# Optimization experiments

Hardware: AMD Instinct MI355X
Metric: run time of the kernel (lower is better)

Reference implementation:

```python
import jax, jax.numpy as jnp
import numpy as np

B, T, C, H = 2, 4096, 512, 8
HD = C // H  # head_dim = 64


def setup_inputs() -> dict:
    key = jax.random.key(0)
    ks = jax.random.split(key, 5)
    s = 0.02
    return {
        "x": jax.random.normal(ks[0], (B, T, C), dtype=jnp.float32),
        "Wqkv": jax.random.normal(ks[1], (C, 3 * C), dtype=jnp.float32) * s,
        "bqkv": jax.random.normal(ks[2], (3 * C,), dtype=jnp.float32) * s,
        "Wproj": jax.random.normal(ks[3], (C, C), dtype=jnp.float32) * s,
        "bproj": jax.random.normal(ks[4], (C,), dtype=jnp.float32) * s,
    }


def reference(x, Wqkv, bqkv, Wproj, bproj):
    b, t, c = x.shape
    qkv = x @ Wqkv + bqkv                      # [B,T,3C]
    q, k, v = jnp.split(qkv, 3, axis=-1)
    # [B,T,C] -> [B,H,T,HD]
    q = q.reshape(b, t, H, HD).transpose(0, 2, 1, 3)
    k = k.reshape(b, t, H, HD).transpose(0, 2, 1, 3)
    v = v.reshape(b, t, H, HD).transpose(0, 2, 1, 3)
    att = jnp.einsum("bhqd,bhkd->bhqk", q, k) / jnp.sqrt(jnp.float32(HD))
    causal = jnp.tril(jnp.ones((t, t), dtype=bool))
    att = jnp.where(causal, att, -jnp.inf)
    att = jax.nn.softmax(att, axis=-1)
    y = jnp.einsum("bhqk,bhkd->bhqd", att, v)  # [B,H,T,HD]
    y = y.transpose(0, 2, 1, 3).reshape(b, t, c)
    return y @ Wproj + bproj
```

## Files before the change

### kernel.cpp

```cpp
#include <hip/hip_runtime.h>
#include <math.h>

#define NB 2
#define NT 4096
#define NC 512
#define NH 8
#define ND 64
#define N3C (3*NC)

typedef __attribute__((ext_vector_type(8))) __bf16 bf16x8;
typedef __attribute__((ext_vector_type(4))) __bf16 bf16x4;
typedef __attribute__((ext_vector_type(4))) float  f32x4;

__global__ __launch_bounds__(256) void cvt_bf16_kernel(
    const float* __restrict__ x, __bf16* __restrict__ xb, int n)
{
    const int i = (blockIdx.x * 256 + threadIdx.x) << 3;
    if (i < n) {
        float4 a = *(const float4*)(x + i);
        float4 b = *(const float4*)(x + i + 4);
        bf16x8 o;
        o[0] = (__bf16)a.x; o[1] = (__bf16)a.y; o[2] = (__bf16)a.z; o[3] = (__bf16)a.w;
        o[4] = (__bf16)b.x; o[5] = (__bf16)b.y; o[6] = (__bf16)b.z; o[7] = (__bf16)b.w;
        *(bf16x8*)(xb + i) = o;
    }
}

__global__ __launch_bounds__(256) void transpose_cvt_kernel(
    const float* __restrict__ W, __bf16* __restrict__ Wt, int K, int N)
{
    __shared__ float T[64][65];
    const int n0 = blockIdx.x << 6, k0 = blockIdx.y << 6;
    const int tx = threadIdx.x & 15, ty = threadIdx.x >> 4;
#pragma unroll
    for (int i = 0; i < 4; ++i) {
        const int r = ty + (i << 4);
        float4 v = *(const float4*)(W + (size_t)(k0 + r) * N + n0 + (tx << 2));
        T[r][(tx << 2) + 0] = v.x;
        T[r][(tx << 2) + 1] = v.y;
        T[r][(tx << 2) + 2] = v.z;
        T[r][(tx << 2) + 3] = v.w;
    }
    __syncthreads();
#pragma unroll
    for (int i = 0; i < 4; ++i) {
        const int nr = ty + (i << 4);
        bf16x4 o;
        o[0] = (__bf16)T[(tx << 2) + 0][nr];
        o[1] = (__bf16)T[(tx << 2) + 1][nr];
        o[2] = (__bf16)T[(tx << 2) + 2][nr];
        o[3] = (__bf16)T[(tx << 2) + 3][nr];
        *(bf16x4*)(Wt + (size_t)(n0 + nr) * K + k0 + (tx << 2)) = o;
    }
}

__global__ __launch_bounds__(256) void gemm_bf16_kernel(
    const __bf16* __restrict__ A, const __bf16* __restrict__ Bt,
    const float* __restrict__ bias, void* __restrict__ Cout,
    int M, int N, int K, int out_bf16)
{
    __shared__ __bf16 As[128][40];
    __shared__ __bf16 Bs[128][40];

    const int tid  = threadIdx.x;
    const int w    = tid >> 6, lane = tid & 63;
    const int g    = lane >> 4, n = lane & 15;
    const int wr   = (w >> 1) << 6;
    const int wc   = (w & 1) << 6;
    const int m0   = blockIdx.y << 7, n0 = blockIdx.x << 7;

    const int sr = tid >> 1;
    const int sh = (tid & 1) << 4;
    const __bf16* ap = A  + (size_t)(m0 + sr) * K + sh;
    const __bf16* bp = Bt + (size_t)(n0 + sr) * K + sh;

    f32x4 acc[4][4];
#pragma unroll
    for (int i = 0; i < 4; ++i)
#pragma unroll
        for (int j = 0; j < 4; ++j) acc[i][j] = (f32x4){0.f, 0.f, 0.f, 0.f};

    bf16x8 a0 = *(const bf16x8*)ap;
    bf16x8 a1 = *(const bf16x8*)(ap + 8);
    bf16x8 b0 = *(const bf16x8*)bp;
    bf16x8 b1 = *(const bf16x8*)(bp + 8);

    const int ksteps = K >> 5;
    for (int ks = 0; ks < ksteps; ++ks) {
        __syncthreads();
        *(bf16x8*)&As[sr][sh]     = a0;
        *(bf16x8*)&As[sr][sh + 8] = a1;
        *(bf16x8*)&Bs[sr][sh]     = b0;
        *(bf16x8*)&Bs[sr][sh + 8] = b1;
        __syncthreads();

        if (ks + 1 < ksteps) {
            const int ko = (ks + 1) << 5;
            a0 = *(const bf16x8*)(ap + ko);
            a1 = *(const bf16x8*)(ap + ko + 8);
            b0 = *(const bf16x8*)(bp + ko);
            b1 = *(const bf16x8*)(bp + ko + 8);
        }

        bf16x8 af[4], bf[4];
#pragma unroll
        for (int i = 0; i < 4; ++i) {
            af[i] = *(const bf16x8*)&As[wr + (i << 4) + n][g << 3];
            bf[i] = *(const bf16x8*)&Bs[wc + (i << 4) + n][g << 3];
        }
#pragma unroll
        for (int i = 0; i < 4; ++i)
#pragma unroll
            for (int j = 0; j < 4; ++j)
                acc[i][j] = __builtin_amdgcn_mfma_f32_16x16x32_bf16(af[i], bf[j], acc[i][j], 0, 0, 0);
    }

#pragma unroll
    for (int j = 0; j < 4; ++j) {
        const int colg = n0 + wc + (j << 4) + n;
        const float bb = bias[colg];
#pragma unroll
        for (int i = 0; i < 4; ++i) {
#pragma unroll
            for (int reg = 0; reg < 4; ++reg) {
                const int rowg = m0 + wr + (i << 4) + (g << 2) + reg;
                const float v = acc[i][j][reg] + bb;
                if (out_bf16)
                    ((__bf16*)Cout)[(size_t)rowg * N + colg] = (__bf16)v;
                else
                    ((float*)Cout)[(size_t)rowg * N + colg] = v;
            }
        }
    }
}

__global__ __launch_bounds__(512) void attn_kernel(
    const __bf16* __restrict__ qkv, __bf16* __restrict__ out)
{
    __shared__ __align__(16) unsigned char SMEM[36352];
    __bf16 (*QPs)[72] = (__bf16(*)[72])SMEM;
    __bf16 (*Ks)[72]  = (__bf16(*)[72])(SMEM + 18432);
    __bf16 (*Vt)[68]  = (__bf16(*)[68])(SMEM + 27648);

    const int tid  = threadIdx.x;
    const int xi   = blockIdx.x;
    const int bh   = blockIdx.y;
    const int qb   = (bh < 8) ? (31 - xi) : xi;
    const int b    = bh >> 3, h = bh & 7;
    const int qr0  = qb << 7;
    const size_t base = (size_t)b * NT * N3C;
    const int col  = h * ND;

    const int w    = tid >> 6;
    const int lane = tid & 63;
    const int g    = lane >> 4;
    const int n    = lane & 15;
    const int qg   = w >> 1;
    const int kh   = w & 1;
    const int qrow0 = qg << 5;
    const int kcol0 = kh << 5;
    const int sw   = (g ^ (n >> 2)) << 3;

    const int kr = tid >> 3;
    const int kc = (tid & 7) << 3;
    const int vd = lane;
    const int vk = w << 2;

    const __bf16* kptr = qkv + base + NC + col + kc;
    const __bf16* vptr = qkv + base + 2 * NC + col + vd;

#pragma unroll
    for (int i = 0; i < 2; ++i) {
        const int r = kr + (i << 6);
        bf16x8 v = *(const bf16x8*)(qkv + base + (size_t)(qr0 + r) * N3C + col + kc);
        bf16x8 q;
#pragma unroll
        for (int j = 0; j < 8; ++j) q[j] = (__bf16)(0.125f * (float)v[j]);
        *(bf16x8*)&QPs[r][kc] = q;
    }
    __syncthreads();

    bf16x8 qf[2][2];
#pragma unroll
    for (int qt = 0; qt < 2; ++qt)
#pragma unroll
        for (int hh = 0; hh < 2; ++hh)
            qf[qt][hh] = *(const bf16x8*)&QPs[qrow0 + (qt << 4) + n][(hh << 5) + (g << 3)];

    bf16x8 ones;
#pragma unroll
    for (int j = 0; j < 8; ++j) ones[j] = (__bf16)1.0f;

    f32x4 O[2][4];
#pragma unroll
    for (int qt = 0; qt < 2; ++qt)
#pragma unroll
        for (int dt = 0; dt < 4; ++dt) O[qt][dt] = (f32x4){0.f, 0.f, 0.f, 0.f};
    f32x4 L[2] = {{0.f,0.f,0.f,0.f},{0.f,0.f,0.f,0.f}};

    bf16x8 kreg = *(const bf16x8*)(kptr + (size_t)kr * N3C);
    __bf16 vreg[8];
#pragma unroll
    for (int j = 0; j < 4; ++j) {
        vreg[j]     = vptr[(size_t)(vk + j) * N3C];
        vreg[4 + j] = vptr[(size_t)(vk + 32 + j) * N3C];
    }

    const int ntiles = (qb << 1) + 2;
    for (int jt = 0; jt < ntiles; ++jt) {
        __syncthreads();
        *(bf16x8*)&Ks[kr][kc] = kreg;
        {
            bf16x4 va, vb;
#pragma unroll
            for (int j = 0; j < 4; ++j) { va[j] = vreg[j]; vb[j] = vreg[4 + j]; }
            *(bf16x4*)&Vt[vd][vk]      = va;
            *(bf16x4*)&Vt[vd][vk + 32] = vb;
        }
        __syncthreads();

        if (jt + 1 < ntiles) {
            const int kr1 = (jt + 1) << 6;
            kreg = *(const bf16x8*)(kptr + (size_t)(kr1 + kr) * N3C);
#pragma unroll
            for (int j = 0; j < 4; ++j) {
                vreg[j]     = vptr[(size_t)(kr1 + vk + j) * N3C];
                vreg[4 + j] = vptr[(size_t)(kr1 + vk + 32 + j) * N3C];
            }
        }

        f32x4 S[2][2];
#pragma unroll
        for (int t = 0; t < 2; ++t) {
            const bf16x8 k0 = *(const bf16x8*)&Ks[kcol0 + (t << 4) + n][(g << 3)];
            const bf16x8 k1 = *(const bf16x8*)&Ks[kcol0 + (t << 4) + n][32 + (g << 3)];
#pragma unroll
            for (int qt = 0; qt < 2; ++qt) {
                f32x4 a = {0.f, 0.f, 0.f, 0.f};
                a = __builtin_amdgcn_mfma_f32_16x16x32_bf16(qf[qt][0], k0, a, 0, 0, 0);
                a = __builtin_amdgcn_mfma_f32_16x16x32_bf16(qf[qt][1], k1, a, 0, 0, 0);
                S[qt][t] = a;
            }
        }

        if (jt >= (qb << 1)) {
#pragma unroll
            for (int qt = 0; qt < 2; ++qt)
#pragma unroll
                for (int t = 0; t < 2; ++t)
#pragma unroll
                    for (int reg = 0; reg < 4; ++reg) {
                        const int kg = (jt << 6) + kcol0 + (t << 4) + n;
                        const int qgl = qr0 + qrow0 + (qt << 4) + (g << 2) + reg;
                        if (kg > qgl) S[qt][t][reg] = -INFINITY;
                    }
        }

#pragma unroll
        for (int qt = 0; qt < 2; ++qt)
#pragma unroll
            for (int t = 0; t < 2; ++t)
#pragma unroll
                for (int reg = 0; reg < 4; ++reg)
                    QPs[qrow0 + (qt << 4) + (g << 2) + reg]
                       [kcol0 + (((t << 4) + n) ^ (g << 3))] =
                        (__bf16)__expf(S[qt][t][reg]);

        bf16x8 vf[4];
#pragma unroll
        for (int dt = 0; dt < 4; ++dt) {
            const int vr = (dt << 4) + n;
            const bf16x4 lo = *(const bf16x4*)&Vt[vr][kcol0 + (g << 3)];
            const bf16x4 hi = *(const bf16x4*)&Vt[vr][kcol0 + (g << 3) + 4];
#pragma unroll
            for (int j = 0; j < 4; ++j) { vf[dt][j] = lo[j]; vf[dt][4 + j] = hi[j]; }
        }

#pragma unroll
        for (int qt = 0; qt < 2; ++qt) {
            const bf16x8 p = *(const bf16x8*)&QPs[qrow0 + (qt << 4) + n][kcol0 + sw];
            L[qt] = __builtin_amdgcn_mfma_f32_16x16x32_bf16(p, ones, L[qt], 0, 0, 0);
#pragma unroll
            for (int dt = 0; dt < 4; ++dt)
                O[qt][dt] = __builtin_amdgcn_mfma_f32_16x16x32_bf16(p, vf[dt], O[qt][dt], 0, 0, 0);
        }
    }

    __syncthreads();
    float* red = (float*)SMEM;
    if (kh == 1) {
#pragma unroll
        for (int qt = 0; qt < 2; ++qt)
#pragma unroll
            for (int reg = 0; reg < 4; ++reg) {
                const int qlx = qrow0 + (qt << 4) + (g << 2) + reg;
#pragma unroll
                for (int dt = 0; dt < 4; ++dt)
                    red[qlx * 64 + (dt << 4) + n] = O[qt][dt][reg];
                if (n == 0) red[8192 + qlx] = L[qt][reg];
            }
    }
    __syncthreads();
    if (kh == 0) {
#pragma unroll
        for (int qt = 0; qt < 2; ++qt)
#pragma unroll
            for (int reg = 0; reg < 4; ++reg) {
                const int qlx = qrow0 + (qt << 4) + (g << 2) + reg;
                const float inv = 1.0f / (L[qt][reg] + red[8192 + qlx]);
                const size_t row = (size_t)b * NT + qr0 + qlx;
#pragma unroll
                for (int dt = 0; dt < 4; ++dt)
                    out[row * NC + col + (dt << 4) + n] =
                        (__bf16)((O[qt][dt][reg] + red[qlx * 64 + (dt << 4) + n]) * inv);
            }
    }
}

extern "C" void kernel_launch(void* const* d_in, const int* in_sizes, int n_in,
                              void* d_out, int out_size, void* d_ws, size_t ws_size,
                              hipStream_t stream)
{
    const float* x     = (const float*)d_in[0];
    const float* Wqkv  = (const float*)d_in[1];
    const float* bqkv  = (const float*)d_in[2];
    const float* Wproj = (const float*)d_in[3];
    const float* bproj = (const float*)d_in[4];
    float* out = (float*)d_out;

    char* ws = (char*)d_ws;
    __bf16* xb     = (__bf16*)(ws);
    __bf16* qkvb   = (__bf16*)(ws + 8388608);
    __bf16* attb   = (__bf16*)(ws + 33554432);
    __bf16* wqkvt  = (__bf16*)(ws + 41943040);
    __bf16* wprojt = (__bf16*)(ws + 43515904);

    cvt_bf16_kernel<<<dim3(2048), dim3(256), 0, stream>>>(x, xb, NB * NT * NC);
    transpose_cvt_kernel<<<dim3(N3C / 64, NC / 64), dim3(256), 0, stream>>>(
        Wqkv, wqkvt, NC, N3C);
    transpose_cvt_kernel<<<dim3(NC / 64, NC / 64), dim3(256), 0, stream>>>(
        Wproj, wprojt, NC, NC);

    gemm_bf16_kernel<<<dim3(N3C / 128, (NB * NT) / 128), dim3(256), 0, stream>>>(
        xb, wqkvt, bqkv, qkvb, NB * NT, N3C, NC, 1);

    attn_kernel<<<dim3(NT / 128, NB * NH), dim3(512), 0, stream>>>(qkvb, attb);

    gemm_bf16_kernel<<<dim3(NC / 128, (NB * NT) / 128), dim3(256), 0, stream>>>(
        attb, wprojt, bproj, out, NB * NT, NC, NC, 0);
}
```

Baseline: 205.9 us.

## Fuse x bf16 conversion into QKV GEMM and merge weight prep kernels

Removes the standalone fp32-to-bf16 conversion of x by having the QKV GEMM load fp32 A tiles and convert them while staging into shared memory. It also merges the two weight transpose-convert launches into one prep kernel. The aim is to save two launches and the write and re-read of the bf16 x buffer. In exchange, the QKV GEMM reads x as fp32 twelve times over (once per N-tile column), doubling its A-side global traffic.

```diff
diff --git a/kernel.cpp b/kernel.cpp
--- a/kernel.cpp
+++ b/kernel.cpp
@@ -12,25 +12,17 @@
 typedef __attribute__((ext_vector_type(4))) __bf16 bf16x4;
 typedef __attribute__((ext_vector_type(4))) float  f32x4;
 
-__global__ __launch_bounds__(256) void cvt_bf16_kernel(
-    const float* __restrict__ x, __bf16* __restrict__ xb, int n)
-{
-    const int i = (blockIdx.x * 256 + threadIdx.x) << 3;
-    if (i < n) {
-        float4 a = *(const float4*)(x + i);
-        float4 b = *(const float4*)(x + i + 4);
-        bf16x8 o;
-        o[0] = (__bf16)a.x; o[1] = (__bf16)a.y; o[2] = (__bf16)a.z; o[3] = (__bf16)a.w;
-        o[4] = (__bf16)b.x; o[5] = (__bf16)b.y; o[6] = (__bf16)b.z; o[7] = (__bf16)b.w;
-        *(bf16x8*)(xb + i) = o;
-    }
-}
-
-__global__ __launch_bounds__(256) void transpose_cvt_kernel(
-    const float* __restrict__ W, __bf16* __restrict__ Wt, int K, int N)
+__global__ __launch_bounds__(256) void prep_kernel(
+    const float* __restrict__ Wqkv, const float* __restrict__ Wproj,
+    __bf16* __restrict__ wqkvt, __bf16* __restrict__ wprojt)
 {
     __shared__ float T[64][65];
-    const int n0 = blockIdx.x << 6, k0 = blockIdx.y << 6;
+    int id = blockIdx.x;
+    const float* W; __bf16* Wt; int N, n0, k0;
+    if (id < 192) { W = Wqkv;  Wt = wqkvt;  N = N3C; n0 = (id % 24) << 6; k0 = (id / 24) << 6; }
+    else { id -= 192; W = Wproj; Wt = wprojt; N = NC;  n0 = (id & 7) << 6;  k0 = (id >> 3) << 6; }
+    const int K = NC;
+
     const int tx = threadIdx.x & 15, ty = threadIdx.x >> 4;
 #pragma unroll
     for (int i = 0; i < 4; ++i) {
@@ -54,8 +46,9 @@
     }
 }
 
+template<bool AF32>
 __global__ __launch_bounds__(256) void gemm_bf16_kernel(
-    const __bf16* __restrict__ A, const __bf16* __restrict__ Bt,
+    const void* __restrict__ Aptr, const __bf16* __restrict__ Bt,
     const float* __restrict__ bias, void* __restrict__ Cout,
     int M, int N, int K, int out_bf16)
 {
@@ -71,8 +64,9 @@
 
     const int sr = tid >> 1;
     const int sh = (tid & 1) << 4;
-    const __bf16* ap = A  + (size_t)(m0 + sr) * K + sh;
-    const __bf16* bp = Bt + (size_t)(n0 + sr) * K + sh;
+    const __bf16* ap_h = (const __bf16*)Aptr + (size_t)(m0 + sr) * K + sh;
+    const float*  ap_f = (const float*) Aptr + (size_t)(m0 + sr) * K + sh;
+    const __bf16* bp   = Bt + (size_t)(n0 + sr) * K + sh;
 
     f32x4 acc[4][4];
 #pragma unroll
@@ -80,24 +74,50 @@
 #pragma unroll
         for (int j = 0; j < 4; ++j) acc[i][j] = (f32x4){0.f, 0.f, 0.f, 0.f};
 
-    bf16x8 a0 = *(const bf16x8*)ap;
-    bf16x8 a1 = *(const bf16x8*)(ap + 8);
+    bf16x8 a0, a1;
+    float4 f0, f1, f2, f3;
+    if constexpr (AF32) {
+        f0 = *(const float4*)(ap_f);
+        f1 = *(const float4*)(ap_f + 4);
+        f2 = *(const float4*)(ap_f + 8);
+        f3 = *(const float4*)(ap_f + 12);
+    } else {
+        a0 = *(const bf16x8*)ap_h;
+        a1 = *(const bf16x8*)(ap_h + 8);
+    }
     bf16x8 b0 = *(const bf16x8*)bp;
     bf16x8 b1 = *(const bf16x8*)(bp + 8);
 
     const int ksteps = K >> 5;
     for (int ks = 0; ks < ksteps; ++ks) {
         __syncthreads();
-        *(bf16x8*)&As[sr][sh]     = a0;
-        *(bf16x8*)&As[sr][sh + 8] = a1;
+        if constexpr (AF32) {
+            bf16x8 c0, c1;
+            c0[0] = (__bf16)f0.x; c0[1] = (__bf16)f0.y; c0[2] = (__bf16)f0.z; c0[3] = (__bf16)f0.w;
+            c0[4] = (__bf16)f1.x; c0[5] = (__bf16)f1.y; c0[6] = (__bf16)f1.z; c0[7] = (__bf16)f1.w;
+            c1[0] = (__bf16)f2.x; c1[1] = (__bf16)f2.y; c1[2] = (__bf16)f2.z; c1[3] = (__bf16)f2.w;
+            c1[4] = (__bf16)f3.x; c1[5] = (__bf16)f3.y; c1[6] = (__bf16)f3.z; c1[7] = (__bf16)f3.w;
+            *(bf16x8*)&As[sr][sh]     = c0;
+            *(bf16x8*)&As[sr][sh + 8] = c1;
+        } else {
+            *(bf16x8*)&As[sr][sh]     = a0;
+            *(bf16x8*)&As[sr][sh + 8] = a1;
+        }
         *(bf16x8*)&Bs[sr][sh]     = b0;
         *(bf16x8*)&Bs[sr][sh + 8] = b1;
         __syncthreads();
 
         if (ks + 1 < ksteps) {
             const int ko = (ks + 1) << 5;
-            a0 = *(const bf16x8*)(ap + ko);
-            a1 = *(const bf16x8*)(ap + ko + 8);
+            if constexpr (AF32) {
+                f0 = *(const float4*)(ap_f + ko);
+                f1 = *(const float4*)(ap_f + ko + 4);
+                f2 = *(const float4*)(ap_f + ko + 8);
+                f3 = *(const float4*)(ap_f + ko + 12);
+            } else {
+                a0 = *(const bf16x8*)(ap_h + ko);
+                a1 = *(const bf16x8*)(ap_h + ko + 8);
+            }
             b0 = *(const bf16x8*)(bp + ko);
             b1 = *(const bf16x8*)(bp + ko + 8);
         }
@@ -329,23 +349,18 @@
     float* out = (float*)d_out;
 
     char* ws = (char*)d_ws;
-    __bf16* xb     = (__bf16*)(ws);
-    __bf16* qkvb   = (__bf16*)(ws + 8388608);
-    __bf16* attb   = (__bf16*)(ws + 33554432);
-    __bf16* wqkvt  = (__bf16*)(ws + 41943040);
-    __bf16* wprojt = (__bf16*)(ws + 43515904);
-
-    cvt_bf16_kernel<<<dim3(2048), dim3(256), 0, stream>>>(x, xb, NB * NT * NC);
-    transpose_cvt_kernel<<<dim3(N3C / 64, NC / 64), dim3(256), 0, stream>>>(
-        Wqkv, wqkvt, NC, N3C);
-    transpose_cvt_kernel<<<dim3(NC / 64, NC / 64), dim3(256), 0, stream>>>(
-        Wproj, wprojt, NC, NC);
-
-    gemm_bf16_kernel<<<dim3(N3C / 128, (NB * NT) / 128), dim3(256), 0, stream>>>(
-        xb, wqkvt, bqkv, qkvb, NB * NT, N3C, NC, 1);
+    __bf16* qkvb   = (__bf16*)(ws);
+    __bf16* attb   = (__bf16*)(ws + 25165824);
+    __bf16* wqkvt  = (__bf16*)(ws + 33554432);
+    __bf16* wprojt = (__bf16*)(ws + 35127296);
+
+    prep_kernel<<<dim3(256), dim3(256), 0, stream>>>(Wqkv, Wproj, wqkvt, wprojt);
+
+    gemm_bf16_kernel<true><<<dim3(N3C / 128, (NB * NT) / 128), dim3(256), 0, stream>>>(
+        x, wqkvt, bqkv, qkvb, NB * NT, N3C, NC, 1);
 
     attn_kernel<<<dim3(NT / 128, NB * NH), dim3(512), 0, stream>>>(qkvb, attb);
 
-    gemm_bf16_kernel<<<dim3(NC / 128, (NB * NT) / 128), dim3(256), 0, stream>>>(
+    gemm_bf16_kernel<false><<<dim3(NC / 128, (NB * NT) / 128), dim3(256), 0, stream>>>(
         attb, wprojt, bproj, out, NB * NT, NC, NC, 0);
 }
```

New measurement: 206.8 us. No clear change (+0.4%).

## Use direct global-to-LDS loads with XOR-swizzled tiles in GEMMs, merge weight prep

Applied to the files above, without the earlier changes.

The GEMM kernel now stages A and B tiles with global_load_lds, writing straight into LDS without going through registers. Tiles use an XOR swizzle in place of padding to avoid bank conflicts, and the K step is doubled to 64. The two weight-transpose launches are merged into one kernel, and the output projection uses a 64-row tile to put more blocks on the grid. In exchange, the register prefetch overlap is lost: loads are issued and synchronised within each step, with no double buffering.

```diff
diff --git a/kernel.cpp b/kernel.cpp
--- a/kernel.cpp
+++ b/kernel.cpp
@@ -11,6 +11,12 @@
 typedef __attribute__((ext_vector_type(8))) __bf16 bf16x8;
 typedef __attribute__((ext_vector_type(4))) __bf16 bf16x4;
 typedef __attribute__((ext_vector_type(4))) float  f32x4;
+
+__device__ __forceinline__ void load_lds16(const __bf16* g, __bf16* l) {
+    __builtin_amdgcn_global_load_lds(
+        (const __attribute__((address_space(1))) void*)g,
+        (__attribute__((address_space(3))) void*)l, 16, 0, 0);
+}
 
 __global__ __launch_bounds__(256) void cvt_bf16_kernel(
     const float* __restrict__ x, __bf16* __restrict__ xb, int n)
@@ -26,11 +32,17 @@
     }
 }
 
-__global__ __launch_bounds__(256) void transpose_cvt_kernel(
-    const float* __restrict__ W, __bf16* __restrict__ Wt, int K, int N)
+__global__ __launch_bounds__(256) void prep_kernel(
+    const float* __restrict__ Wqkv, const float* __restrict__ Wproj,
+    __bf16* __restrict__ wqkvt, __bf16* __restrict__ wprojt)
 {
     __shared__ float T[64][65];
-    const int n0 = blockIdx.x << 6, k0 = blockIdx.y << 6;
+    int id = blockIdx.x;
+    const float* W; __bf16* Wt; int N, n0, k0;
+    if (id < 192) { W = Wqkv;  Wt = wqkvt;  N = N3C; n0 = (id % 24) << 6; k0 = (id / 24) << 6; }
+    else { id -= 192; W = Wproj; Wt = wprojt; N = NC;  n0 = (id & 7) << 6;  k0 = (id >> 3) << 6; }
+    const int K = NC;
+
     const int tx = threadIdx.x & 15, ty = threadIdx.x >> 4;
 #pragma unroll
     for (int i = 0; i < 4; ++i) {
@@ -54,65 +66,77 @@
     }
 }
 
-__global__ __launch_bounds__(256) void gemm_bf16_kernel(
+template<int BM>
+__global__ __launch_bounds__(256) void gemm_glds_kernel(
     const __bf16* __restrict__ A, const __bf16* __restrict__ Bt,
     const float* __restrict__ bias, void* __restrict__ Cout,
     int M, int N, int K, int out_bf16)
 {
-    __shared__ __bf16 As[128][40];
-    __shared__ __bf16 Bs[128][40];
+    constexpr int IT = BM / 32;
+    constexpr int AI = BM / 32;
+    __shared__ __align__(16) __bf16 As[BM * 64];
+    __shared__ __align__(16) __bf16 Bs[128 * 64];
 
     const int tid  = threadIdx.x;
     const int w    = tid >> 6, lane = tid & 63;
     const int g    = lane >> 4, n = lane & 15;
-    const int wr   = (w >> 1) << 6;
+    const int n7   = n & 7;
+    const int wr   = (w >> 1) * (BM / 2);
     const int wc   = (w & 1) << 6;
-    const int m0   = blockIdx.y << 7, n0 = blockIdx.x << 7;
-
-    const int sr = tid >> 1;
-    const int sh = (tid & 1) << 4;
-    const __bf16* ap = A  + (size_t)(m0 + sr) * K + sh;
-    const __bf16* bp = Bt + (size_t)(n0 + sr) * K + sh;
-
-    f32x4 acc[4][4];
-#pragma unroll
-    for (int i = 0; i < 4; ++i)
+    const int m0   = blockIdx.y * BM, n0 = blockIdx.x << 7;
+
+    const __bf16* ag[AI]; __bf16* al[AI];
+#pragma unroll
+    for (int q = 0; q < AI; ++q) {
+        const int G = w * (BM * 2) + q * 64 + lane;
+        const int r = G >> 3, pg = G & 7, kg = pg ^ (r & 7);
+        ag[q] = A + (size_t)(m0 + r) * K + (kg << 3);
+        al[q] = As + ((w * (BM * 2) + q * 64) << 3);
+    }
+    const __bf16* bg[4]; __bf16* bl[4];
+#pragma unroll
+    for (int q = 0; q < 4; ++q) {
+        const int G = w * 256 + q * 64 + lane;
+        const int r = G >> 3, pg = G & 7, kg = pg ^ (r & 7);
+        bg[q] = Bt + (size_t)(n0 + r) * K + (kg << 3);
+        bl[q] = Bs + ((w * 256 + q * 64) << 3);
+    }
+
+    f32x4 acc[IT][4];
+#pragma unroll
+    for (int i = 0; i < IT; ++i)
 #pragma unroll
         for (int j = 0; j < 4; ++j) acc[i][j] = (f32x4){0.f, 0.f, 0.f, 0.f};
 
-    bf16x8 a0 = *(const bf16x8*)ap;
-    bf16x8 a1 = *(const bf16x8*)(ap + 8);
-    bf16x8 b0 = *(const bf16x8*)bp;
-    bf16x8 b1 = *(const bf16x8*)(bp + 8);
-
-    const int ksteps = K >> 5;
+    const int ksteps = K >> 6;
     for (int ks = 0; ks < ksteps; ++ks) {
         __syncthreads();
-        *(bf16x8*)&As[sr][sh]     = a0;
-        *(bf16x8*)&As[sr][sh + 8] = a1;
-        *(bf16x8*)&Bs[sr][sh]     = b0;
-        *(bf16x8*)&Bs[sr][sh + 8] = b1;
+        const int ko = ks << 6;
+#pragma unroll
+        for (int q = 0; q < AI; ++q) load_lds16(ag[q] + ko, al[q]);
+#pragma unroll
+        for (int q = 0; q < 4;  ++q) load_lds16(bg[q] + ko, bl[q]);
         __syncthreads();
 
-        if (ks + 1 < ksteps) {
-            const int ko = (ks + 1) << 5;
-            a0 = *(const bf16x8*)(ap + ko);
-            a1 = *(const bf16x8*)(ap + ko + 8);
-            b0 = *(const bf16x8*)(bp + ko);
-            b1 = *(const bf16x8*)(bp + ko + 8);
-        }
-
-        bf16x8 af[4], bf[4];
-#pragma unroll
-        for (int i = 0; i < 4; ++i) {
-            af[i] = *(const bf16x8*)&As[wr + (i << 4) + n][g << 3];
-            bf[i] = *(const bf16x8*)&Bs[wc + (i << 4) + n][g << 3];
-        }
-#pragma unroll
-        for (int i = 0; i < 4; ++i)
-#pragma unroll
-            for (int j = 0; j < 4; ++j)
-                acc[i][j] = __builtin_amdgcn_mfma_f32_16x16x32_bf16(af[i], bf[j], acc[i][j], 0, 0, 0);
+#pragma unroll
+        for (int s = 0; s < 2; ++s) {
+            bf16x8 af[IT], bf[4];
+#pragma unroll
+            for (int i = 0; i < IT; ++i) {
+                const int row = wr + (i << 4) + n;
+                af[i] = *(const bf16x8*)&As[(row << 6) + ((((s << 2) + g) ^ n7) << 3)];
+            }
+#pragma unroll
+            for (int j = 0; j < 4; ++j) {
+                const int row = wc + (j << 4) + n;
+                bf[j] = *(const bf16x8*)&Bs[(row << 6) + ((((s << 2) + g) ^ n7) << 3)];
+            }
+#pragma unroll
+            for (int i = 0; i < IT; ++i)
+#pragma unroll
+                for (int j = 0; j < 4; ++j)
+                    acc[i][j] = __builtin_amdgcn_mfma_f32_16x16x32_bf16(af[i], bf[j], acc[i][j], 0, 0, 0);
+        }
     }
 
 #pragma unroll
@@ -120,7 +144,7 @@
         const int colg = n0 + wc + (j << 4) + n;
         const float bb = bias[colg];
 #pragma unroll
-        for (int i = 0; i < 4; ++i) {
+        for (int i = 0; i < IT; ++i) {
 #pragma unroll
             for (int reg = 0; reg < 4; ++reg) {
                 const int rowg = m0 + wr + (i << 4) + (g << 2) + reg;
@@ -336,16 +360,13 @@
     __bf16* wprojt = (__bf16*)(ws + 43515904);
 
     cvt_bf16_kernel<<<dim3(2048), dim3(256), 0, stream>>>(x, xb, NB * NT * NC);
-    transpose_cvt_kernel<<<dim3(N3C / 64, NC / 64), dim3(256), 0, stream>>>(
-        Wqkv, wqkvt, NC, N3C);
-    transpose_cvt_kernel<<<dim3(NC / 64, NC / 64), dim3(256), 0, stream>>>(
-        Wproj, wprojt, NC, NC);
-
-    gemm_bf16_kernel<<<dim3(N3C / 128, (NB * NT) / 128), dim3(256), 0, stream>>>(
+    prep_kernel<<<dim3(256), dim3(256), 0, stream>>>(Wqkv, Wproj, wqkvt, wprojt);
+
+    gemm_glds_kernel<128><<<dim3(N3C / 128, (NB * NT) / 128), dim3(256), 0, stream>>>(
         xb, wqkvt, bqkv, qkvb, NB * NT, N3C, NC, 1);
 
     attn_kernel<<<dim3(NT / 128, NB * NH), dim3(512), 0, stream>>>(qkvb, attb);
 
-    gemm_bf16_kernel<<<dim3(NC / 128, (NB * NT) / 128), dim3(256), 0, stream>>>(
+    gemm_glds_kernel<64><<<dim3(NC / 128, (NB * NT) / 64), dim3(256), 0, stream>>>(
         attb, wprojt, bproj, out, NB * NT, NC, NC, 0);
 }
```

Result: faster. 197.0 us (-4.4%).
